# Kernel tuning notes

Hardware: AMD Instinct MI355X
Metric: run time of the kernel (lower is better)

Reference implementation:

```python
import jax, jax.numpy as jnp
import numpy as np
from jax import lax

WINDOW = 11
C1 = (0.01 * 1) ** 2
C2 = (0.03 * 1) ** 2


def setup_inputs() -> dict:
    key = jax.random.key(0)
    kx, ky = jax.random.split(key)
    x = jax.random.uniform(kx, (8, 3, 512, 512), dtype=jnp.float32)
    y = jax.random.uniform(ky, (8, 3, 512, 512), dtype=jnp.float32)
    return {"x": x, "y": y}


def _window_sum(a):
    # sum over every overlapping WINDOW x WINDOW patch (stride 1, valid)
    return lax.reduce_window(a, 0.0, lax.add,
                             (1, 1, WINDOW, WINDOW),
                             (1, 1, 1, 1), 'VALID')


def reference(x, y):
    # x, y: [B, C, H, W] images in [0, 1]
    n = float(WINDOW * WINDOW)
    sx = _window_sum(x)
    sy = _window_sum(y)
    sxx = _window_sum(x * x)
    syy = _window_sum(y * y)
    sxy = _window_sum(x * y)
    mx = sx / n
    my = sy / n
    # unbiased variance / covariance (matches torch var(unbiased=True) and
    # the bessel-corrected covariance in the original)
    vx = (sxx - n * mx * mx) / (n - 1.0)
    vy = (syy - n * my * my) / (n - 1.0)
    cov = (sxy - n * mx * my) / (n - 1.0)
    ssim = (2.0 * mx * my + C1) * (2.0 * cov + C2) / (
        (mx * mx + my * my + C1) * (vx + vy + C2))
    # original averages over windows (dim 0) and channels (dim 2) -> per-batch
    return (1.0 - ssim.mean(axis=(1, 2, 3))) / 2.0
```

## Files before the change

### kernel.cpp

```cpp
#include <hip/hip_runtime.h>

#define WINDOW 11
#define H 512
#define W 512
#define OH 502
#define OW 502
#define NCH 3
#define BATCH 8
#define RSTRIPE 33
#define NSTRIPES 16
#define NGRP 5
#define GRPW 118
#define WAVES_PER_IMG (NSTRIPES * NGRP)
#define NWAVES (BATCH * NCH * WAVES_PER_IMG)
#define WAVES_PER_BATCH (NCH * WAVES_PER_IMG)
#define NXCD 8
#define CHUNK (NWAVES / NXCD)

#define NPIX_PER_BATCH (3.0f * 502.0f * 502.0f)

typedef float v2f __attribute__((ext_vector_type(2)));

__global__ __launch_bounds__(64) void ssim_main(const float* __restrict__ x,
                                                const float* __restrict__ y,
                                                float* __restrict__ partials) {
    const int lane = threadIdx.x & 63;

    const int wg    = blockIdx.x;
    const int w_lin = (wg % NXCD) * CHUNK + wg / NXCD;

    const int img = w_lin / WAVES_PER_IMG;
    const int rem = w_lin % WAVES_PER_IMG;
    const int grp = rem / NSTRIPES;
    const int rs  = rem % NSTRIPES;

    const int i0 = rs * RSTRIPE;
    const int i1 = min(i0 + RSTRIPE, OH);
    const int cstart = grp * GRPW;
    const int outw   = min(GRPW, OW - cstart);
    const int c0 = min(cstart + 2 * lane, W - 2);
    const bool tapActive = (2 * lane < outw);

    const float* __restrict__ xc = x + (size_t)img * H * W + c0;
    const float* __restrict__ yc = y + (size_t)img * H * W + c0;

    const int s1 = lane + 1, s2 = lane + 2, s4 = lane + 4, s5 = lane + 5;

    v2f fx[11], fy[11];
    v2f Qx = 0.f, Qy = 0.f, Qz = 0.f, Qw = 0.f;
#pragma unroll
    for (int r = 0; r < WINDOW; ++r) {
        v2f a = *(const v2f*)(xc + (size_t)(i0 + r) * W);
        v2f b = *(const v2f*)(yc + (size_t)(i0 + r) * W);
        fx[r] = a; fy[r] = b;
        Qx += a;
        Qy += b;
        Qz += a * a + b * b;
        Qw += a * b;
    }

    v2f nx, ny;
#define LDNEW(j) do {                                                \
        int jc_ = min((j), H - 1);                                   \
        nx = *(const v2f*)(xc + (size_t)jc_ * W);                    \
        ny = *(const v2f*)(yc + (size_t)jc_ * W);                    \
    } while (0)

#define SLIDE(u) do {                                                 \
        Qx += nx - fx[u];                                             \
        Qy += ny - fy[u];                                             \
        Qz += nx * nx + ny * ny - fx[u] * fx[u] - fy[u] * fy[u];      \
        Qw += nx * ny - fx[u] * fy[u];                                \
        fx[u] = nx; fy[u] = ny;                                       \
    } while (0)

    float acc = 0.f;

#define LADDER(T, q0, q1, We, Wo) do {                                \
        float U1 = T + __shfl(T, s1, 64);                             \
        float U2 = U1 + __shfl(U1, s2, 64);                           \
        float S5 = U2 + __shfl(T, s4, 64);                            \
        float S6 = S5 + __shfl(T, s5, 64);                            \
        We = S5 + __shfl(q0, s5, 64);                                 \
        Wo = S6 - T + q1;                                             \
    } while (0)

#define COMPUTE(rowActive) do {                                               \
        float Tx = Qx.x + Qx.y, Ty = Qy.x + Qy.y;                             \
        float Tz = Qz.x + Qz.y, Tw = Qw.x + Qw.y;                             \
        float Wex, Wox, Wey, Woy, Wez, Woz, Wew, Wow;                         \
        LADDER(Tx, Qx.x, Qx.y, Wex, Wox);                                     \
        LADDER(Ty, Qy.x, Qy.y, Wey, Woy);                                     \
        LADDER(Tz, Qz.x, Qz.y, Wez, Woz);                                     \
        LADDER(Tw, Qw.x, Qw.y, Wew, Wow);                                     \
        v2f Wx = {Wex, Wox}, Wy = {Wey, Woy};                                 \
        v2f Wz = {Wez, Woz}, Ww = {Wew, Wow};                                 \
                             \
        v2f mx  = Wx * (1.0f / 121.0f);                                       \
        v2f my  = Wy * (1.0f / 121.0f);                                       \
        v2f mxy = mx * my;                                                    \
        v2f m2  = mx * mx + my * my;                                          \
        v2f cov = (Ww - 121.0f * mxy) * (1.0f / 120.0f);                      \
        v2f vv  = (Wz - 121.0f * m2)  * (1.0f / 120.0f);                      \
        v2f num = (2.0f * mxy + 1e-4f) * (2.0f * cov + 9e-4f);                \
        v2f den = (m2 + 1e-4f) * (vv + 9e-4f);                                \
        float r = num.x * __builtin_amdgcn_rcpf(den.x)                        \
                + num.y * __builtin_amdgcn_rcpf(den.y);                       \
        acc += (tapActive & (rowActive)) ? r : 0.f;                           \
    } while (0)

    LDNEW(i0 + WINDOW);
    for (int base = i0; base < i1; base += 11) {
#pragma unroll
        for (int u = 0; u < 11; ++u) {
            const int i = base + u;
            COMPUTE(i < i1);
            SLIDE(u);
            LDNEW(i + WINDOW + 1);
        }
    }

    for (int off = 32; off > 0; off >>= 1)
        acc += __shfl_down(acc, off, 64);
    if (lane == 0) partials[w_lin] = acc;
}

__global__ __launch_bounds__(256) void ssim_reduce(const float* __restrict__ partials,
                                                   float* __restrict__ out) {
    const int b = blockIdx.x;
    const int t = threadIdx.x;
    float s = 0.f;
    if (t < WAVES_PER_BATCH)
        s = partials[b * WAVES_PER_BATCH + t];
    for (int off = 32; off > 0; off >>= 1)
        s += __shfl_down(s, off, 64);
    __shared__ float red[4];
    int wid = t >> 6, lane = t & 63;
    if (lane == 0) red[wid] = s;
    __syncthreads();
    if (t == 0) {
        float tot = (red[0] + red[1]) + (red[2] + red[3]);
        out[b] = (1.0f - tot / NPIX_PER_BATCH) * 0.5f;
    }
}

extern "C" void kernel_launch(void* const* d_in, const int* in_sizes, int n_in,
                              void* d_out, int out_size, void* d_ws, size_t ws_size,
                              hipStream_t stream) {
    const float* x = (const float*)d_in[0];
    const float* y = (const float*)d_in[1];
    float* out      = (float*)d_out;
    float* partials = (float*)d_ws;

    ssim_main<<<NWAVES, 64, 0, stream>>>(x, y, partials);
    ssim_reduce<<<BATCH, 256, 0, stream>>>(partials, out);
}
```

Baseline: 28.87 us.

## Replace shuffle ladder with DPP prefix scan and shrink row stripes to 11

Computes the 11-wide horizontal window sums from an inclusive wave prefix scan built on DPP row/broadcast ops, with a single shuffle by 5 lanes, instead of the shuffle ladder. This trades several ds_bpermute shuffles per quantity for cheap DPP adds. It also cuts the row stripe from 33 to 11 rows, roughly tripling the number of waves to raise occupancy and parallelism. The cost is more redundant 11-row window priming per output row. The reduce kernel now loops because partials per batch exceed 256.

Result: faster. 25.81 us (-10.6%).

```diff
diff --git a/kernel.cpp b/kernel.cpp
--- a/kernel.cpp
+++ b/kernel.cpp
@@ -7,8 +7,8 @@
 #define OW 502
 #define NCH 3
 #define BATCH 8
-#define RSTRIPE 33
-#define NSTRIPES 16
+#define RSTRIPE 11
+#define NSTRIPES 46
 #define NGRP 5
 #define GRPW 118
 #define WAVES_PER_IMG (NSTRIPES * NGRP)
@@ -20,6 +20,22 @@
 #define NPIX_PER_BATCH (3.0f * 502.0f * 502.0f)
 
 typedef float v2f __attribute__((ext_vector_type(2)));
+
+template <int CTRL, int RM>
+__device__ __forceinline__ float scan_step(float x) {
+    int s = __builtin_amdgcn_update_dpp(0, __builtin_bit_cast(int, x),
+                                        CTRL, RM, 0xf, false);
+    return x + __builtin_bit_cast(float, s);
+}
+__device__ __forceinline__ float wave_iscan(float x) {
+    x = scan_step<0x111, 0xf>(x);
+    x = scan_step<0x112, 0xf>(x);
+    x = scan_step<0x114, 0xf>(x);
+    x = scan_step<0x118, 0xf>(x);
+    x = scan_step<0x142, 0xa>(x);
+    x = scan_step<0x143, 0xc>(x);
+    return x;
+}
 
 __global__ __launch_bounds__(64) void ssim_main(const float* __restrict__ x,
                                                 const float* __restrict__ y,
@@ -43,8 +59,6 @@
 
     const float* __restrict__ xc = x + (size_t)img * H * W + c0;
     const float* __restrict__ yc = y + (size_t)img * H * W + c0;
-
-    const int s1 = lane + 1, s2 = lane + 2, s4 = lane + 4, s5 = lane + 5;
 
     v2f fx[11], fy[11];
     v2f Qx = 0.f, Qy = 0.f, Qz = 0.f, Qw = 0.f;
@@ -76,25 +90,20 @@
 
     float acc = 0.f;
 
-#define LADDER(T, q0, q1, We, Wo) do {                                \
-        float U1 = T + __shfl(T, s1, 64);                             \
-        float U2 = U1 + __shfl(U1, s2, 64);                           \
-        float S5 = U2 + __shfl(T, s4, 64);                            \
-        float S6 = S5 + __shfl(T, s5, 64);                            \
-        We = S5 + __shfl(q0, s5, 64);                                 \
-        Wo = S6 - T + q1;                                             \
-    } while (0)
-
 #define COMPUTE(rowActive) do {                                               \
         float Tx = Qx.x + Qx.y, Ty = Qy.x + Qy.y;                             \
         float Tz = Qz.x + Qz.y, Tw = Qw.x + Qw.y;                             \
-        float Wex, Wox, Wey, Woy, Wez, Woz, Wew, Wow;                         \
-        LADDER(Tx, Qx.x, Qx.y, Wex, Wox);                                     \
-        LADDER(Ty, Qy.x, Qy.y, Wey, Woy);                                     \
-        LADDER(Tz, Qz.x, Qz.y, Wez, Woz);                                     \
-        LADDER(Tw, Qw.x, Qw.y, Wew, Wow);                                     \
-        v2f Wx = {Wex, Wox}, Wy = {Wey, Woy};                                 \
-        v2f Wz = {Wez, Woz}, Ww = {Wew, Wow};                                 \
+        float Sx = wave_iscan(Tx), Sy = wave_iscan(Ty);                       \
+        float Sz = wave_iscan(Tz), Sw = wave_iscan(Tw);                       \
+        int src = lane + 5;                                                   \
+        float Ax = __shfl(Sx, src, 64), Ay = __shfl(Sy, src, 64);             \
+        float Az = __shfl(Sz, src, 64), Aw = __shfl(Sw, src, 64);             \
+        float Bx = __shfl(Qx.y, src, 64), By = __shfl(Qy.y, src, 64);         \
+        float Bz = __shfl(Qz.y, src, 64), Bw = __shfl(Qw.y, src, 64);         \
+        v2f Wx = {Ax - Bx - Sx + Tx, Ax - Sx + Qx.y};                         \
+        v2f Wy = {Ay - By - Sy + Ty, Ay - Sy + Qy.y};                         \
+        v2f Wz = {Az - Bz - Sz + Tz, Az - Sz + Qz.y};                         \
+        v2f Ww = {Aw - Bw - Sw + Tw, Aw - Sw + Qw.y};                         \
                              \
         v2f mx  = Wx * (1.0f / 121.0f);                                       \
         v2f my  = Wy * (1.0f / 121.0f);                                       \
@@ -110,14 +119,12 @@
     } while (0)
 
     LDNEW(i0 + WINDOW);
-    for (int base = i0; base < i1; base += 11) {
 #pragma unroll
-        for (int u = 0; u < 11; ++u) {
-            const int i = base + u;
-            COMPUTE(i < i1);
-            SLIDE(u);
-            LDNEW(i + WINDOW + 1);
-        }
+    for (int u = 0; u < 11; ++u) {
+        const int i = i0 + u;
+        COMPUTE(i < i1);
+        SLIDE(u);
+        LDNEW(i + WINDOW + 1);
     }
 
     for (int off = 32; off > 0; off >>= 1)
@@ -130,8 +137,8 @@
     const int b = blockIdx.x;
     const int t = threadIdx.x;
     float s = 0.f;
-    if (t < WAVES_PER_BATCH)
-        s = partials[b * WAVES_PER_BATCH + t];
+    for (int k = t; k < WAVES_PER_BATCH; k += 256)
+        s += partials[b * WAVES_PER_BATCH + k];
     for (int off = 32; off > 0; off >>= 1)
         s += __shfl_down(s, off, 64);
     __shared__ float red[4];
```
